# Optimization experiments

Measured on AMD Instinct MI355X. Metric: run time of the kernel, lower is better.

Reference implementation:

```python
import jax, jax.numpy as jnp
import numpy as np

LN_EPS = 1e-5

def setup_inputs() -> dict:
    key = jax.random.key(0)
    ks = jax.random.split(key, 6)
    N, CD, CC, CF = 500000, 64, 96, 128
    return {
        "x_detial": jax.random.normal(ks[0], (N, CD), dtype=jnp.float32),
        "x_context": jax.random.normal(ks[1], (N, CC), dtype=jnp.float32),
        "W_detial": jax.random.normal(ks[2], (CD, CF), dtype=jnp.float32) * 0.05,
        "W_context": jax.random.normal(ks[3], (CC, CF), dtype=jnp.float32) * 0.05,
        "W_gate1": jax.random.normal(ks[4], (CD + CC, CF // 2), dtype=jnp.float32) * 0.05,
        "ln_gamma": jnp.ones((CF // 2,), dtype=jnp.float32),
        "ln_beta": jnp.zeros((CF // 2,), dtype=jnp.float32),
        "W_gate2": jax.random.normal(ks[5], (CF // 2, 1), dtype=jnp.float32) * 0.05,
    }

def _layer_norm(x, gamma, beta):
    mu = jnp.mean(x, axis=-1, keepdims=True)
    var = jnp.mean(jnp.square(x - mu), axis=-1, keepdims=True)
    return (x - mu) * jax.lax.rsqrt(var + LN_EPS) * gamma + beta

def reference(x_detial, x_context, W_detial, W_context, W_gate1, ln_gamma, ln_beta, W_gate2):
    # gate path: 1x1 subm conv == per-point linear on [N, C] features
    concat = jnp.concatenate([x_detial, x_context], axis=1)        # [N, CD+CC]
    h = jnp.matmul(concat, W_gate1)                                 # [N, CF//2]
    h = jax.nn.relu(_layer_norm(h, ln_gamma, ln_beta))
    gate = jax.nn.sigmoid(jnp.matmul(h, W_gate2))                   # [N, 1]
    detail_aligned = jnp.matmul(x_detial, W_detial)                 # [N, CF]
    context_aligned = jnp.matmul(x_context, W_context)              # [N, CF]
    return (1.0 - gate) * context_aligned + gate * detail_aligned   # [N, CF]
```

## Files before the change

kernel.cpp:

```cpp
#include <hip/hip_runtime.h>
#include <hip/hip_bf16.h>
#include <math.h>


namespace {

typedef __attribute__((ext_vector_type(8))) short short8;
typedef __attribute__((ext_vector_type(4))) float f32x4;

constexpr int CD = 64, CC = 96, CH = 64, CF = 128;
constexpr int NFG1 = 20;
constexpr int NFCB = 40;
constexpr int NFRAG = NFG1 + NFCB;
constexpr int WCHUNKS = NFCB * 512 * 2 / 16;

__device__ inline short bf16_of(float f) {
  __hip_bfloat16 h = __float2bfloat16(f);
  return *reinterpret_cast<short*>(&h);
}

__global__ void convert_weights(const float* __restrict__ Wd,
                                const float* __restrict__ Wc,
                                const float* __restrict__ Wg1,
                                short* __restrict__ ws) {
  const int t = blockIdx.x * 256 + threadIdx.x;
  if (t >= 64 * NFRAG) return;
  const int frag = t >> 6, l = t & 63;
  const int cidx = l & 15, kb = l >> 4;
  float v[8];
  if (frag < NFG1) {
    const int ks = frag >> 2, nt = frag & 3;
    const int n = nt * 16 + cidx, k0 = ks * 32 + kb * 8;
    #pragma unroll
    for (int j = 0; j < 8; ++j) v[j] = Wg1[(k0 + j) * CH + n];
  } else {
    const int f2 = frag - NFG1;
    const int ks = f2 >> 3, nt = f2 & 7;
    const int n = nt * 16 + cidx, k0 = ks * 32 + kb * 8;
    #pragma unroll
    for (int j = 0; j < 8; ++j) {
      const int k = k0 + j;
      v[j] = (k < CD) ? Wd[k * CF + n] : Wc[(k - CD) * CF + n];
    }
  }
  short8 o;
  #pragma unroll
  for (int j = 0; j < 8; ++j) o[j] = bf16_of(v[j]);
  *reinterpret_cast<short8*>(ws + frag * 512 + l * 8) = o;
}

__global__ __launch_bounds__(512, 4)
void gate_fusion_mfma(const float* __restrict__ xd,
                      const float* __restrict__ xc,
                      const float* __restrict__ gma,
                      const float* __restrict__ bta,
                      const float* __restrict__ Wg2,
                      const short* __restrict__ wf,
                      float* __restrict__ out, int N) {
  __shared__ short wlds[NFCB * 512];

  const int tid  = threadIdx.x;
  const int lane = tid & 63;
  const int wv   = tid >> 6;
  const int r0   = blockIdx.x * 128 + wv * 16;
  const int cidx = lane & 15;
  const int kb   = lane >> 4;
  const bool active = (r0 < N);

  f32x4 buf[5][2];
  if (active) {
    const size_t row = (size_t)(r0 + cidx);
    const float* rd = xd + row * CD + kb * 8;
    const float* rc = xc + row * CC + kb * 8;
    #pragma unroll
    for (int ks = 0; ks < 5; ++ks) {
      const float* p = (ks < 2) ? (rd + ks * 32) : (rc + (ks - 2) * 32);
      buf[ks][0] = *reinterpret_cast<const f32x4*>(p);
      buf[ks][1] = *reinterpret_cast<const f32x4*>(p + 4);
    }
  }

  {
    const short* wsrc = wf + NFG1 * 512;
    #pragma unroll
    for (int it = 0; it < WCHUNKS / 512; ++it) {
      const int c = tid + it * 512;
      short8 v = *reinterpret_cast<const short8*>(wsrc + (size_t)c * 8);
      *reinterpret_cast<short8*>(&wlds[c * 8]) = v;
    }
  }
  __syncthreads();
  if (!active) return;

  float gmv[4], btv[4], w2v[4];
  #pragma unroll
  for (int nt = 0; nt < 4; ++nt) {
    const int c = nt * 16 + cidx;
    gmv[nt] = gma[c]; btv[nt] = bta[c]; w2v[nt] = Wg2[c];
  }

  short8 xf[5];
  #pragma unroll
  for (int ks = 0; ks < 5; ++ks) {
    short8 f;
    #pragma unroll
    for (int j = 0; j < 4; ++j) {
      f[j]     = bf16_of(buf[ks][0][j]);
      f[4 + j] = bf16_of(buf[ks][1][j]);
    }
    xf[ks] = f;
  }

  const f32x4 vzero = {0.f, 0.f, 0.f, 0.f};
  f32x4 acc1[4];
  #pragma unroll
  for (int nt = 0; nt < 4; ++nt) acc1[nt] = vzero;

  #pragma unroll
  for (int ks = 0; ks < 5; ++ks) {
    short8 bg[4];
    #pragma unroll
    for (int nt = 0; nt < 4; ++nt)
      bg[nt] = *reinterpret_cast<const short8*>(wf + (ks * 4 + nt) * 512 + lane * 8);
    #pragma unroll
    for (int nt = 0; nt < 4; ++nt)
      acc1[nt] = __builtin_amdgcn_mfma_f32_16x16x32_bf16(
          xf[ks], bg[nt], acc1[nt], 0, 0, 0);
  }

  float gate[4];
  {
    float s[4], q[4];
    #pragma unroll
    for (int r = 0; r < 4; ++r) {
      s[r] = 0.f; q[r] = 0.f;
      #pragma unroll
      for (int nt = 0; nt < 4; ++nt) {
        const float c = acc1[nt][r];
        s[r] += c; q[r] += c * c;
      }
    }
    #pragma unroll
    for (int m = 1; m < 16; m <<= 1)
      #pragma unroll
      for (int r = 0; r < 4; ++r) {
        s[r] += __shfl_xor(s[r], m, 64);
        q[r] += __shfl_xor(q[r], m, 64);
      }
    float p[4];
    #pragma unroll
    for (int r = 0; r < 4; ++r) {
      const float mu  = s[r] * (1.f / CH);
      const float var = q[r] * (1.f / CH) - mu * mu;
      const float rsd = rsqrtf(var + 1e-5f);
      float pp = 0.f;
      #pragma unroll
      for (int nt = 0; nt < 4; ++nt) {
        const float h = fmaxf((acc1[nt][r] - mu) * rsd * gmv[nt] + btv[nt], 0.f);
        pp += h * w2v[nt];
      }
      p[r] = pp;
    }
    #pragma unroll
    for (int m = 1; m < 16; m <<= 1)
      #pragma unroll
      for (int r = 0; r < 4; ++r) p[r] += __shfl_xor(p[r], m, 64);
    #pragma unroll
    for (int r = 0; r < 4; ++r) gate[r] = 1.f / (1.f + expf(-p[r]));
  }

  #pragma unroll
  for (int q = 0; q < 4; ++q) {
    f32x4 aD[2], aC[2];
    #pragma unroll
    for (int nt = 0; nt < 2; ++nt) { aD[nt] = vzero; aC[nt] = vzero; }

    #pragma unroll
    for (int ks = 0; ks < 5; ++ks) {
      short8 bg[2];
      #pragma unroll
      for (int nt = 0; nt < 2; ++nt)
        bg[nt] = *reinterpret_cast<const short8*>(
            &wlds[(ks * 8 + q * 2 + nt) * 512 + lane * 8]);
      if (ks < 2) {
        #pragma unroll
        for (int nt = 0; nt < 2; ++nt)
          aD[nt] = __builtin_amdgcn_mfma_f32_16x16x32_bf16(
              xf[ks], bg[nt], aD[nt], 0, 0, 0);
      } else {
        #pragma unroll
        for (int nt = 0; nt < 2; ++nt)
          aC[nt] = __builtin_amdgcn_mfma_f32_16x16x32_bf16(
              xf[ks], bg[nt], aC[nt], 0, 0, 0);
      }
    }

    {
      const size_t rowb = (size_t)r0 + kb * 4;
      #pragma unroll
      for (int nt = 0; nt < 2; ++nt) {
        #pragma unroll
        for (int r = 0; r < 4; ++r) {
          const float g = gate[r];
          const float o = fmaf(g, aD[nt][r] - aC[nt][r], aC[nt][r]);
          out[(rowb + r) * CF + (q * 2 + nt) * 16 + cidx] = o;
        }
      }
    }
  }
}

}

extern "C" void kernel_launch(void* const* d_in, const int* in_sizes, int n_in,
                              void* d_out, int out_size, void* d_ws, size_t ws_size,
                              hipStream_t stream) {
  const float* xd  = (const float*)d_in[0];
  const float* xc  = (const float*)d_in[1];
  const float* Wd  = (const float*)d_in[2];
  const float* Wc  = (const float*)d_in[3];
  const float* Wg1 = (const float*)d_in[4];
  const float* gma = (const float*)d_in[5];
  const float* bta = (const float*)d_in[6];
  const float* Wg2 = (const float*)d_in[7];
  float* out = (float*)d_out;
  short* ws  = (short*)d_ws;

  const int N = in_sizes[0] / CD;

  convert_weights<<<dim3(15), dim3(256), 0, stream>>>(Wd, Wc, Wg1, ws);

  const int nblk = (N + 127) / 128;
  gate_fusion_mfma<<<dim3(nblk), dim3(512), 0, stream>>>(
      xd, xc, gma, bta, Wg2, ws, out, N);
}
```

Before: 134.7 us.

## Persistent blocks with double-buffered async global-to-LDS input staging

Replaces one-shot 512-thread blocks with 1024 persistent 128-thread blocks, each looping over 32-row chunks. Each chunk's inputs are prefetched into double-buffered, XOR-swizzled LDS with global_load_lds DMA while the previous chunk is computed. Weight fragments now come straight from global memory (L1/L2 cached) instead of being copied into LDS by every block. This aims to overlap input loads with MFMA work and drop the per-block weight copy. It assumes N is divisible by 32 and adds register pressure from holding all weight fragments.

```diff
diff --git a/kernel.cpp b/kernel.cpp
--- a/kernel.cpp
+++ b/kernel.cpp
@@ -10,9 +10,11 @@
 
 constexpr int CD = 64, CC = 96, CH = 64, CF = 128;
 constexpr int NFG1 = 20;
-constexpr int NFCB = 40;
-constexpr int NFRAG = NFG1 + NFCB;
-constexpr int WCHUNKS = NFCB * 512 * 2 / 16;
+constexpr int NFRAG = 60;
+constexpr int RPC  = 32;
+constexpr int DBYT = RPC * CD * 4;
+constexpr int CBYT = RPC * CC * 4;
+constexpr int CHKB = DBYT + CBYT;
 
 __device__ inline short bf16_of(float f) {
   __hip_bfloat16 h = __float2bfloat16(f);
@@ -49,48 +51,59 @@
   *reinterpret_cast<short8*>(ws + frag * 512 + l * 8) = o;
 }
 
-__global__ __launch_bounds__(512, 4)
+typedef const __attribute__((address_space(1))) unsigned int GU;
+typedef __attribute__((address_space(3))) unsigned int LU;
+
+__device__ inline void dma16(const void* g, void* l) {
+  __builtin_amdgcn_global_load_lds((GU*)g, (LU*)l, 16, 0, 0);
+}
+
+__device__ inline void stage_chunk(const char* __restrict__ xdb,
+                                   const char* __restrict__ xcb,
+                                   int row0, char* buf, int tid) {
+  const char* gD = xdb + (size_t)row0 * (CD * 4);
+  char* wub0 = buf + ((tid & ~63) * 16);
+  #pragma unroll
+  for (int it = 0; it < 4; ++it) {
+    const int pg  = it * 128 + tid;
+    const int row = pg >> 4;
+    const int lg  = pg ^ (row & 7);
+    dma16(gD + (size_t)lg * 16, wub0 + it * 128 * 16);
+  }
+  const char* gC = xcb + (size_t)row0 * (CC * 4);
+  char* wub1 = buf + DBYT + ((tid & ~63) * 16);
+  #pragma unroll
+  for (int it = 0; it < 6; ++it) {
+    const int pg  = it * 128 + tid;
+    const int row = pg / 24;
+    const int u   = pg - row * 24;
+    const int lg  = row * 24 + (u ^ (row & 7));
+    dma16(gC + (size_t)lg * 16, wub1 + it * 128 * 16);
+  }
+}
+
+__global__ __launch_bounds__(128, 2)
 void gate_fusion_mfma(const float* __restrict__ xd,
                       const float* __restrict__ xc,
                       const float* __restrict__ gma,
                       const float* __restrict__ bta,
                       const float* __restrict__ Wg2,
                       const short* __restrict__ wf,
-                      float* __restrict__ out, int N) {
-  __shared__ short wlds[NFCB * 512];
+                      float* __restrict__ out,
+                      int q, int rr) {
+  __shared__ char lds[2][CHKB];
 
   const int tid  = threadIdx.x;
   const int lane = tid & 63;
   const int wv   = tid >> 6;
-  const int r0   = blockIdx.x * 128 + wv * 16;
   const int cidx = lane & 15;
   const int kb   = lane >> 4;
-  const bool active = (r0 < N);
-
-  f32x4 buf[5][2];
-  if (active) {
-    const size_t row = (size_t)(r0 + cidx);
-    const float* rd = xd + row * CD + kb * 8;
-    const float* rc = xc + row * CC + kb * 8;
-    #pragma unroll
-    for (int ks = 0; ks < 5; ++ks) {
-      const float* p = (ks < 2) ? (rd + ks * 32) : (rc + (ks - 2) * 32);
-      buf[ks][0] = *reinterpret_cast<const f32x4*>(p);
-      buf[ks][1] = *reinterpret_cast<const f32x4*>(p + 4);
-    }
-  }
-
-  {
-    const short* wsrc = wf + NFG1 * 512;
-    #pragma unroll
-    for (int it = 0; it < WCHUNKS / 512; ++it) {
-      const int c = tid + it * 512;
-      short8 v = *reinterpret_cast<const short8*>(wsrc + (size_t)c * 8);
-      *reinterpret_cast<short8*>(&wlds[c * 8]) = v;
-    }
-  }
-  __syncthreads();
-  if (!active) return;
+  const int b    = blockIdx.x;
+  const int start = b * q + (b < rr ? b : rr);
+  const int cnt   = q + (b < rr ? 1 : 0);
+
+  const char* xdb = (const char*)xd;
+  const char* xcb = (const char*)xc;
 
   float gmv[4], btv[4], w2v[4];
   #pragma unroll
@@ -99,114 +112,139 @@
     gmv[nt] = gma[c]; btv[nt] = bta[c]; w2v[nt] = Wg2[c];
   }
 
-  short8 xf[5];
-  #pragma unroll
-  for (int ks = 0; ks < 5; ++ks) {
-    short8 f;
-    #pragma unroll
-    for (int j = 0; j < 4; ++j) {
-      f[j]     = bf16_of(buf[ks][0][j]);
-      f[4 + j] = bf16_of(buf[ks][1][j]);
-    }
-    xf[ks] = f;
-  }
-
   const f32x4 vzero = {0.f, 0.f, 0.f, 0.f};
-  f32x4 acc1[4];
-  #pragma unroll
-  for (int nt = 0; nt < 4; ++nt) acc1[nt] = vzero;
-
-  #pragma unroll
-  for (int ks = 0; ks < 5; ++ks) {
-    short8 bg[4];
-    #pragma unroll
-    for (int nt = 0; nt < 4; ++nt)
-      bg[nt] = *reinterpret_cast<const short8*>(wf + (ks * 4 + nt) * 512 + lane * 8);
-    #pragma unroll
-    for (int nt = 0; nt < 4; ++nt)
-      acc1[nt] = __builtin_amdgcn_mfma_f32_16x16x32_bf16(
-          xf[ks], bg[nt], acc1[nt], 0, 0, 0);
-  }
-
-  float gate[4];
-  {
-    float s[4], q[4];
-    #pragma unroll
-    for (int r = 0; r < 4; ++r) {
-      s[r] = 0.f; q[r] = 0.f;
-      #pragma unroll
-      for (int nt = 0; nt < 4; ++nt) {
-        const float c = acc1[nt][r];
-        s[r] += c; q[r] += c * c;
-      }
-    }
-    #pragma unroll
-    for (int m = 1; m < 16; m <<= 1)
+  const int lr = wv * 16 + cidx;
+  const int sw = (lr & 7) << 4;
+
+  stage_chunk(xdb, xcb, start * RPC, lds[0], tid);
+  __syncthreads();
+
+  for (int t = 0; t < cnt; ++t) {
+    if (t + 1 < cnt)
+      stage_chunk(xdb, xcb, (start + t + 1) * RPC, lds[(t + 1) & 1], tid);
+
+    char* bD = lds[t & 1];
+    char* bC = lds[t & 1] + DBYT;
+    const int row0 = (start + t) * RPC;
+
+    short8 xf[5];
+    #pragma unroll
+    for (int ks = 0; ks < 5; ++ks) {
+      f32x4 lo, hi;
+      if (ks < 2) {
+        const int base = lr * 256 + ks * 128 + kb * 32;
+        lo = *reinterpret_cast<const f32x4*>(bD + (base ^ sw));
+        hi = *reinterpret_cast<const f32x4*>(bD + ((base + 16) ^ sw));
+      } else {
+        const int base = lr * 384 + (ks - 2) * 128 + kb * 32;
+        lo = *reinterpret_cast<const f32x4*>(bC + (base ^ sw));
+        hi = *reinterpret_cast<const f32x4*>(bC + ((base + 16) ^ sw));
+      }
+      short8 f;
+      #pragma unroll
+      for (int j = 0; j < 4; ++j) { f[j] = bf16_of(lo[j]); f[4 + j] = bf16_of(hi[j]); }
+      xf[ks] = f;
+    }
+
+    short8 wg[5][4];
+    #pragma unroll
+    for (int ks = 0; ks < 5; ++ks)
+      #pragma unroll
+      for (int nt = 0; nt < 4; ++nt)
+        wg[ks][nt] = *reinterpret_cast<const short8*>(wf + (ks * 4 + nt) * 512 + lane * 8);
+
+    f32x4 acc1[4];
+    #pragma unroll
+    for (int nt = 0; nt < 4; ++nt) acc1[nt] = vzero;
+    #pragma unroll
+    for (int ks = 0; ks < 5; ++ks)
+      #pragma unroll
+      for (int nt = 0; nt < 4; ++nt)
+        acc1[nt] = __builtin_amdgcn_mfma_f32_16x16x32_bf16(
+            xf[ks], wg[ks][nt], acc1[nt], 0, 0, 0);
+
+    float gate[4];
+    {
+      float s[4], qq[4];
       #pragma unroll
       for (int r = 0; r < 4; ++r) {
-        s[r] += __shfl_xor(s[r], m, 64);
-        q[r] += __shfl_xor(q[r], m, 64);
-      }
-    float p[4];
-    #pragma unroll
-    for (int r = 0; r < 4; ++r) {
-      const float mu  = s[r] * (1.f / CH);
-      const float var = q[r] * (1.f / CH) - mu * mu;
-      const float rsd = rsqrtf(var + 1e-5f);
-      float pp = 0.f;
-      #pragma unroll
-      for (int nt = 0; nt < 4; ++nt) {
-        const float h = fmaxf((acc1[nt][r] - mu) * rsd * gmv[nt] + btv[nt], 0.f);
-        pp += h * w2v[nt];
-      }
-      p[r] = pp;
-    }
-    #pragma unroll
-    for (int m = 1; m < 16; m <<= 1)
-      #pragma unroll
-      for (int r = 0; r < 4; ++r) p[r] += __shfl_xor(p[r], m, 64);
-    #pragma unroll
-    for (int r = 0; r < 4; ++r) gate[r] = 1.f / (1.f + expf(-p[r]));
-  }
-
-  #pragma unroll
-  for (int q = 0; q < 4; ++q) {
-    f32x4 aD[2], aC[2];
-    #pragma unroll
-    for (int nt = 0; nt < 2; ++nt) { aD[nt] = vzero; aC[nt] = vzero; }
-
-    #pragma unroll
-    for (int ks = 0; ks < 5; ++ks) {
-      short8 bg[2];
-      #pragma unroll
-      for (int nt = 0; nt < 2; ++nt)
-        bg[nt] = *reinterpret_cast<const short8*>(
-            &wlds[(ks * 8 + q * 2 + nt) * 512 + lane * 8]);
-      if (ks < 2) {
+        s[r] = 0.f; qq[r] = 0.f;
+        #pragma unroll
+        for (int nt = 0; nt < 4; ++nt) {
+          const float c = acc1[nt][r];
+          s[r] += c; qq[r] += c * c;
+        }
+      }
+      #pragma unroll
+      for (int m = 1; m < 16; m <<= 1)
+        #pragma unroll
+        for (int r = 0; r < 4; ++r) {
+          s[r]  += __shfl_xor(s[r],  m, 64);
+          qq[r] += __shfl_xor(qq[r], m, 64);
+        }
+      float p[4];
+      #pragma unroll
+      for (int r = 0; r < 4; ++r) {
+        const float mu  = s[r] * (1.f / CH);
+        const float var = qq[r] * (1.f / CH) - mu * mu;
+        const float rsd = rsqrtf(var + 1e-5f);
+        float pp = 0.f;
+        #pragma unroll
+        for (int nt = 0; nt < 4; ++nt) {
+          const float h = fmaxf((acc1[nt][r] - mu) * rsd * gmv[nt] + btv[nt], 0.f);
+          pp += h * w2v[nt];
+        }
+        p[r] = pp;
+      }
+      #pragma unroll
+      for (int m = 1; m < 16; m <<= 1)
+        #pragma unroll
+        for (int r = 0; r < 4; ++r) p[r] += __shfl_xor(p[r], m, 64);
+      #pragma unroll
+      for (int r = 0; r < 4; ++r) gate[r] = 1.f / (1.f + expf(-p[r]));
+    }
+
+    #pragma unroll
+    for (int qs = 0; qs < 4; ++qs) {
+      short8 wb[5][2];
+      #pragma unroll
+      for (int ks = 0; ks < 5; ++ks)
         #pragma unroll
         for (int nt = 0; nt < 2; ++nt)
-          aD[nt] = __builtin_amdgcn_mfma_f32_16x16x32_bf16(
-              xf[ks], bg[nt], aD[nt], 0, 0, 0);
-      } else {
-        #pragma unroll
-        for (int nt = 0; nt < 2; ++nt)
-          aC[nt] = __builtin_amdgcn_mfma_f32_16x16x32_bf16(
-              xf[ks], bg[nt], aC[nt], 0, 0, 0);
-      }
-    }
-
-    {
-      const size_t rowb = (size_t)r0 + kb * 4;
+          wb[ks][nt] = *reinterpret_cast<const short8*>(
+              wf + (NFG1 + ks * 8 + qs * 2 + nt) * 512 + lane * 8);
+
+      f32x4 aD[2], aC[2];
+      #pragma unroll
+      for (int nt = 0; nt < 2; ++nt) { aD[nt] = vzero; aC[nt] = vzero; }
+      #pragma unroll
+      for (int ks = 0; ks < 5; ++ks) {
+        if (ks < 2) {
+          #pragma unroll
+          for (int nt = 0; nt < 2; ++nt)
+            aD[nt] = __builtin_amdgcn_mfma_f32_16x16x32_bf16(
+                xf[ks], wb[ks][nt], aD[nt], 0, 0, 0);
+        } else {
+          #pragma unroll
+          for (int nt = 0; nt < 2; ++nt)
+            aC[nt] = __builtin_amdgcn_mfma_f32_16x16x32_bf16(
+                xf[ks], wb[ks][nt], aC[nt], 0, 0, 0);
+        }
+      }
+
+      const size_t rowb = (size_t)row0 + wv * 16 + kb * 4;
       #pragma unroll
       for (int nt = 0; nt < 2; ++nt) {
         #pragma unroll
         for (int r = 0; r < 4; ++r) {
           const float g = gate[r];
           const float o = fmaf(g, aD[nt][r] - aC[nt][r], aC[nt][r]);
-          out[(rowb + r) * CF + (q * 2 + nt) * 16 + cidx] = o;
-        }
-      }
-    }
+          out[(rowb + r) * CF + (qs * 2 + nt) * 16 + cidx] = o;
+        }
+      }
+    }
+
+    __syncthreads();
   }
 }
 
@@ -227,10 +265,13 @@
   short* ws  = (short*)d_ws;
 
   const int N = in_sizes[0] / CD;
+  const int nChunks = N / RPC;
 
   convert_weights<<<dim3(15), dim3(256), 0, stream>>>(Wd, Wc, Wg1, ws);
 
-  const int nblk = (N + 127) / 128;
-  gate_fusion_mfma<<<dim3(nblk), dim3(512), 0, stream>>>(
-      xd, xc, gma, bta, Wg2, ws, out, N);
-}
+  const int nblk = 1024;
+  const int q  = nChunks / nblk;
+  const int rr = nChunks - q * nblk;
+  gate_fusion_mfma<<<dim3(nblk), dim3(128), 0, stream>>>(
+      xd, xc, gma, bta, Wg2, ws, out, q, rr);
+}
```

Result: slower. 305.3 us (+126.6%).
